# Kernel optimization log

Measured on AMD Instinct MI355X. Metric: run time of the kernel, lower is better.

Reference implementation:

```python
import jax, jax.numpy as jnp
import numpy as np

N_NODES = 100000


def gcn_conv(x, src, dst, W, b, n):
    # PyG GCNConv: add self-loops, symmetric deg^-1/2 normalization,
    # linear transform, gather->scatter-add aggregation, + bias.
    loop = jnp.arange(n, dtype=src.dtype)
    s = jnp.concatenate([src, loop])
    d = jnp.concatenate([dst, loop])
    deg = jax.ops.segment_sum(jnp.ones_like(d, dtype=x.dtype), d, num_segments=n)
    dinv = jnp.where(deg > 0, jax.lax.rsqrt(deg), jnp.zeros_like(deg))
    norm = dinv[s] * dinv[d]            # [E+N]
    h = x @ W                            # [N, out] (transform before propagate)
    msg = h[s] * norm[:, None]           # gather + scale
    out = jax.ops.segment_sum(msg, d, num_segments=n)  # scatter-add to dst
    return out + b


def setup_inputs() -> dict:
    key = jax.random.key(0)
    k = jax.random.split(key, 6)
    n, e, c_in, hid, c_out = N_NODES, 2500000, 5, 32, 1
    x = jax.random.normal(k[0], (n, c_in), dtype=jnp.float32)
    edge_index = jax.random.randint(k[1], (2, e), 0, n, dtype=jnp.int64)
    # Glorot-style init for GCN weights, zero bias (PyG default)
    W1 = jax.random.normal(k[2], (c_in, hid), dtype=jnp.float32) * (1.0 / np.sqrt(c_in))
    b1 = jnp.zeros((hid,), dtype=jnp.float32)
    W2 = jax.random.normal(k[3], (hid, c_out), dtype=jnp.float32) * (1.0 / np.sqrt(hid))
    b2 = jnp.zeros((c_out,), dtype=jnp.float32)
    return {"x": x, "edge_index": edge_index, "W1": W1, "b1": b1, "W2": W2, "b2": b2}


def reference(x, edge_index, W1, b1, W2, b2):
    n = x.shape[0]
    src, dst = edge_index[0], edge_index[1]
    h = jax.nn.relu(gcn_conv(x, src, dst, W1, b1, n))
    # dropout p=0.3 is identity at inference (training=False)
    return jax.nn.sigmoid(gcn_conv(h, src, dst, W2, b2, n))
```

## Files before the change

### kernel.cpp

```cpp
#include <hip/hip_runtime.h>
#include <math.h>


#define NB_SHIFT  8
#define BNODES    256
#define NBK       512
#define CAP       8192
#define CAP_SHIFT 13
#define CHUNK     4888
#define PBLK      512
#define RPT       16

struct SMemP0 {
    int sp[CHUNK];
    unsigned short sb[CHUNK];
    int cnt[NBK], ofs[NBK], cur[NBK], gbase[NBK];
    int wtmp[8];
};
struct SMemP1 {
    int stage2[CAP];
    int ofs[BNODES], cnt[BNODES], cur[BNODES];
    float w1[160], bb1[32], w2[32];
    int wtmp[8];
};
union SMem { SMemP0 p0; SMemP1 p1; };

__device__ __forceinline__ void gbar_arrive(int* bar, int tid) {
    __syncthreads();
    if (tid == 0) {
        __threadfence();
        __hip_atomic_fetch_add(bar, 1, __ATOMIC_RELAXED,
                               __HIP_MEMORY_SCOPE_AGENT);
    }
}
__device__ __forceinline__ void gbar_wait(int* bar, int tgt, int tid) {
    if (tid == 0) {
        while (__hip_atomic_load(bar, __ATOMIC_RELAXED,
                                 __HIP_MEMORY_SCOPE_AGENT) < tgt)
            __builtin_amdgcn_s_sleep(1);
        __threadfence();
    }
    __syncthreads();
}

__global__ __launch_bounds__(PBLK, 4) void k_fused(
        const int* __restrict__ src, const int* __restrict__ dst, int E,
        const float* __restrict__ x,
        const float* __restrict__ W1, const float* __restrict__ b1,
        const float* __restrict__ W2, const float* __restrict__ b2,
        float* __restrict__ out,
        int* __restrict__ pairs, int* __restrict__ bcur, int* __restrict__ gbar,
        float* __restrict__ h2s, float* __restrict__ xs, int n, int nb) {
    __shared__ SMem sm;
    const int tid  = threadIdx.x;
    const int blk  = blockIdx.x;
    const int G    = gridDim.x;
    const int lane = tid & 63, wv = tid >> 6;
    const int nbase = blk << NB_SHIFT;

    {
        int base = blk * CHUNK;
        if (base < E) {
            int m = min(CHUNK, E - base);
            sm.p0.cnt[tid] = 0;
            __syncthreads();
            for (int i = tid; i < m; i += 2 * PBLK) {
                int i1 = i + PBLK;
                int k0 = dst[base + i] >> NB_SHIFT;
                int k1 = (i1 < m) ? (dst[base + i1] >> NB_SHIFT) : -1;
                atomicAdd(&sm.p0.cnt[k0], 1);
                if (k1 >= 0) atomicAdd(&sm.p0.cnt[k1], 1);
            }
            __syncthreads();
            int v = sm.p0.cnt[tid];
            int s = v;
#pragma unroll
            for (int d = 1; d < 64; d <<= 1) {
                int t = __shfl_up(s, d);
                if (lane >= d) s += t;
            }
            if (lane == 63) sm.p0.wtmp[wv] = s;
            __syncthreads();
            if (wv == 0) {
                int t = (lane < 8) ? sm.p0.wtmp[lane] : 0;
#pragma unroll
                for (int d = 1; d < 8; d <<= 1) {
                    int u = __shfl_up(t, d);
                    if (lane >= d) t += u;
                }
                if (lane < 8) sm.p0.wtmp[lane] = t;
            }
            __syncthreads();
            int pre = s + (wv ? sm.p0.wtmp[wv - 1] : 0) - v;
            sm.p0.ofs[tid] = pre;
            sm.p0.cur[tid] = pre;
            sm.p0.gbase[tid] = (tid << CAP_SHIFT)
                             + (v ? atomicAdd(&bcur[tid], v) : 0);
            __syncthreads();
            for (int i = tid; i < m; i += 4 * PBLK) {
                int ia = i + PBLK, ib = i + 2 * PBLK, ic = i + 3 * PBLK;
                int s0 = src[base + i], d0 = dst[base + i];
                int s1 = 0, d1 = 0, s2 = 0, d2 = 0, s3 = 0, d3 = 0;
                if (ia < m) { s1 = src[base + ia]; d1 = dst[base + ia]; }
                if (ib < m) { s2 = src[base + ib]; d2 = dst[base + ib]; }
                if (ic < m) { s3 = src[base + ic]; d3 = dst[base + ic]; }
                int b0 = d0 >> NB_SHIFT;
                int p0 = atomicAdd(&sm.p0.cur[b0], 1);
                sm.p0.sp[p0] = ((d0 & (BNODES - 1)) << 24) | s0;
                sm.p0.sb[p0] = (unsigned short)b0;
                if (ia < m) {
                    int b1k = d1 >> NB_SHIFT;
                    int p1 = atomicAdd(&sm.p0.cur[b1k], 1);
                    sm.p0.sp[p1] = ((d1 & (BNODES - 1)) << 24) | s1;
                    sm.p0.sb[p1] = (unsigned short)b1k;
                }
                if (ib < m) {
                    int b2k = d2 >> NB_SHIFT;
                    int p2 = atomicAdd(&sm.p0.cur[b2k], 1);
                    sm.p0.sp[p2] = ((d2 & (BNODES - 1)) << 24) | s2;
                    sm.p0.sb[p2] = (unsigned short)b2k;
                }
                if (ic < m) {
                    int b3k = d3 >> NB_SHIFT;
                    int p3 = atomicAdd(&sm.p0.cur[b3k], 1);
                    sm.p0.sp[p3] = ((d3 & (BNODES - 1)) << 24) | s3;
                    sm.p0.sb[p3] = (unsigned short)b3k;
                }
            }
            __syncthreads();
            for (int i = tid; i < m; i += PBLK) {
                int b = sm.p0.sb[i];
                pairs[sm.p0.gbase[b] + (i - sm.p0.ofs[b])] = sm.p0.sp[i];
            }
        }
    }
    gbar_arrive(gbar, tid);
    float xr0 = 0.f, xr1 = 0.f, xr2 = 0.f, xr3 = 0.f, xr4 = 0.f;
    if (blk < nb) {
        if (tid < 160) sm.p1.w1[tid] = W1[tid];
        else if (tid < 192) sm.p1.bb1[tid - 160] = b1[tid - 160];
        else if (tid < 224) sm.p1.w2[tid - 192] = W2[tid - 192];
        if (tid < BNODES) {
            sm.p1.cnt[tid] = 0;
            int node = nbase + tid;
            if (node < n) {
                const float* xp = x + (size_t)node * 5;
                xr0 = xp[0]; xr1 = xp[1]; xr2 = xp[2]; xr3 = xp[3]; xr4 = xp[4];
            }
        }
    }
    gbar_wait(gbar, G, tid);

    int nrec = 0;
    int rec[RPT];
    if (blk < nb) {
        int base = blk << CAP_SHIFT;
        int len = min(((volatile int*)bcur)[blk], CAP);
#pragma unroll
        for (int j = 0; j < RPT; ++j) {
            int i = tid + j * PBLK;
            if (i < len) { rec[j] = pairs[base + i]; nrec = j + 1; }
        }
#pragma unroll
        for (int j = 0; j < RPT; ++j)
            if (j < nrec) atomicAdd(&sm.p1.cnt[((unsigned)rec[j]) >> 24], 1);
        __syncthreads();
        int v = (tid < BNODES) ? sm.p1.cnt[tid] : 0;
        int s = v;
#pragma unroll
        for (int d = 1; d < 64; d <<= 1) {
            int t = __shfl_up(s, d);
            if (lane >= d) s += t;
        }
        if (lane == 63 && wv < 4) sm.p1.wtmp[wv] = s;
        __syncthreads();
        if (wv == 0) {
            int t = (lane < 4) ? sm.p1.wtmp[lane] : 0;
#pragma unroll
            for (int d = 1; d < 4; d <<= 1) {
                int u = __shfl_up(t, d);
                if (lane >= d) t += u;
            }
            if (lane < 4) sm.p1.wtmp[lane] = t;
        }
        __syncthreads();
        if (tid < BNODES) {
            int pre = s + (wv ? sm.p1.wtmp[wv - 1] : 0) - v;
            sm.p1.ofs[tid] = pre;
            sm.p1.cur[tid] = pre;
            int node = nbase + tid;
            if (node < n) {
                float di = rsqrtf((float)v + 1.0f);
                float* xo = xs + ((size_t)node << 3);
                xo[0] = xr0 * di; xo[1] = xr1 * di; xo[2] = xr2 * di;
                xo[3] = xr3 * di; xo[4] = xr4 * di;
            }
        }
    }
    gbar_arrive(gbar, tid);
    if (blk < nb) {
#pragma unroll
        for (int j = 0; j < RPT; ++j)
            if (j < nrec) {
                int p = atomicAdd(&sm.p1.cur[((unsigned)rec[j]) >> 24], 1);
                sm.p1.stage2[p] = rec[j] & 0x00FFFFFF;
            }
    }
    gbar_wait(gbar, 2 * G, tid);

    if (blk < nb) {
        int t2 = tid >> 1, half = tid & 1;
        int node = nbase + t2;
        if (node < n) {
            int beg = sm.p1.ofs[t2], dg = sm.p1.cnt[t2];
            float a0 = 0.f, a1 = 0.f, a2 = 0.f, a3 = 0.f, a4 = 0.f;
            if (!half) {
                const float* xo = xs + ((size_t)node << 3);
                a0 = xo[0]; a1 = xo[1]; a2 = xo[2]; a3 = xo[3]; a4 = xo[4];
            }
            for (int e = beg + half; e < beg + dg; e += 2) {
                int sidx = sm.p1.stage2[e];
                const float* xr = xs + ((size_t)sidx << 3);
                float4 q = *(const float4*)xr;
                float q4 = xr[4];
                a0 += q.x; a1 += q.y; a2 += q.z; a3 += q.w; a4 += q4;
            }
            a0 += __shfl_xor(a0, 1); a1 += __shfl_xor(a1, 1);
            a2 += __shfl_xor(a2, 1); a3 += __shfl_xor(a3, 1);
            a4 += __shfl_xor(a4, 1);
            if (!half) {
                float di = rsqrtf((float)dg + 1.0f);
                a0 *= di; a1 *= di; a2 *= di; a3 *= di; a4 *= di;
                float sum = 0.f;
#pragma unroll
                for (int c = 0; c < 32; ++c) {
                    float z = sm.p1.bb1[c] + a0 * sm.p1.w1[c]
                            + a1 * sm.p1.w1[32 + c] + a2 * sm.p1.w1[64 + c]
                            + a3 * sm.p1.w1[96 + c] + a4 * sm.p1.w1[128 + c];
                    sum += fmaxf(z, 0.f) * sm.p1.w2[c];
                }
                h2s[node] = sum * di;
            }
        }
    }
    gbar_arrive(gbar, tid);
    gbar_wait(gbar, 3 * G, tid);

    if (blk < nb) {
        int t2 = tid >> 1, half = tid & 1;
        int node = nbase + t2;
        if (node >= n) return;
        int beg = sm.p1.ofs[t2], dg = sm.p1.cnt[t2];
        float a = 0.f;
        for (int e = beg + half; e < beg + dg; e += 2)
            a += h2s[sm.p1.stage2[e]];
        a += __shfl_xor(a, 1);
        if (!half) {
            float di = rsqrtf((float)dg + 1.0f);
            float vv = di * (a + h2s[node]) + b2[0];
            out[node] = 1.0f / (1.0f + __expf(-vv));
        }
    }
}


__global__ __launch_bounds__(512) void k_part(const int* __restrict__ src,
                                              const int* __restrict__ dst, int E,
                                              int* __restrict__ bcur,
                                              int* __restrict__ pairs) {
    __shared__ int sp[CHUNK];
    __shared__ unsigned short sb[CHUNK];
    __shared__ int cnt[NBK], ofs[NBK], cur[NBK], gbase[NBK];
    int tid = threadIdx.x;
    int base = blockIdx.x * CHUNK;
    int m = min(CHUNK, E - base);

    if (tid < NBK) cnt[tid] = 0;
    __syncthreads();
    for (int i = tid; i < m; i += 2 * 512) {
        int i1 = i + 512;
        int k0 = dst[base + i] >> NB_SHIFT;
        int k1 = (i1 < m) ? (dst[base + i1] >> NB_SHIFT) : -1;
        atomicAdd(&cnt[k0], 1);
        if (k1 >= 0) atomicAdd(&cnt[k1], 1);
    }
    __syncthreads();
    int v = cnt[tid];
    ofs[tid] = v;
    __syncthreads();
    for (int off = 1; off < NBK; off <<= 1) {
        int u = (tid >= off) ? ofs[tid - off] : 0;
        __syncthreads();
        ofs[tid] += u;
        __syncthreads();
    }
    int pre = ofs[tid] - v;
    ofs[tid] = pre;
    cur[tid] = pre;
    gbase[tid] = (tid << CAP_SHIFT) + (v ? atomicAdd(&bcur[tid], v) : 0);
    __syncthreads();
    for (int i = tid; i < m; i += 4 * 512) {
        int ia = i + 512, ib = i + 1024, ic = i + 1536;
        int s0 = src[base + i], d0 = dst[base + i];
        int s1 = 0, d1 = 0, s2 = 0, d2 = 0, s3 = 0, d3 = 0;
        if (ia < m) { s1 = src[base + ia]; d1 = dst[base + ia]; }
        if (ib < m) { s2 = src[base + ib]; d2 = dst[base + ib]; }
        if (ic < m) { s3 = src[base + ic]; d3 = dst[base + ic]; }
        int b0 = d0 >> NB_SHIFT;
        int p0 = atomicAdd(&cur[b0], 1);
        sp[p0] = ((d0 & (BNODES - 1)) << 24) | s0;
        sb[p0] = (unsigned short)b0;
        if (ia < m) {
            int b1 = d1 >> NB_SHIFT;
            int p1 = atomicAdd(&cur[b1], 1);
            sp[p1] = ((d1 & (BNODES - 1)) << 24) | s1;
            sb[p1] = (unsigned short)b1;
        }
        if (ib < m) {
            int b2 = d2 >> NB_SHIFT;
            int p2 = atomicAdd(&cur[b2], 1);
            sp[p2] = ((d2 & (BNODES - 1)) << 24) | s2;
            sb[p2] = (unsigned short)b2;
        }
        if (ic < m) {
            int b3 = d3 >> NB_SHIFT;
            int p3 = atomicAdd(&cur[b3], 1);
            sp[p3] = ((d3 & (BNODES - 1)) << 24) | s3;
            sb[p3] = (unsigned short)b3;
        }
    }
    __syncthreads();
    for (int i = tid; i < m; i += 512) {
        int b = sb[i];
        pairs[gbase[b] + (i - ofs[b])] = sp[i];
    }
}

__global__ __launch_bounds__(512) void k_sorta(const int* __restrict__ pairs,
                                               const int* __restrict__ bcur,
                                               const float* __restrict__ x,
                                               float* __restrict__ dinv,
                                               float* __restrict__ xs,
                                               int* __restrict__ nofs,
                                               int* __restrict__ deg, int n) {
    __shared__ int cnt[BNODES], scn[BNODES];
    int tid = threadIdx.x;
    int b = blockIdx.x;
    int base = b << CAP_SHIFT;
    int len = min(bcur[b], CAP);

    if (tid < BNODES) cnt[tid] = 0;
    __syncthreads();
    for (int i = tid; i < len; i += 512)
        atomicAdd(&cnt[((unsigned)pairs[base + i]) >> 24], 1);
    __syncthreads();
    int v = (tid < BNODES) ? cnt[tid] : 0;
    if (tid < BNODES) scn[tid] = v;
    __syncthreads();
    for (int off = 1; off < BNODES; off <<= 1) {
        int u = (tid < BNODES && tid >= off) ? scn[tid - off] : 0;
        __syncthreads();
        if (tid < BNODES) scn[tid] += u;
        __syncthreads();
    }
    if (tid < BNODES) {
        int node = (b << NB_SHIFT) + tid;
        if (node < n) {
            nofs[node] = base + scn[tid] - v;
            deg[node] = v;
            float di = rsqrtf((float)v + 1.0f);
            dinv[node] = di;
            const float* xr = x + (size_t)node * 5;
            float* xo = xs + ((size_t)node << 3);
#pragma unroll
            for (int k = 0; k < 5; ++k) xo[k] = xr[k] * di;
        }
    }
}

__global__ __launch_bounds__(512) void k_sortagg1(int* __restrict__ pairs,
                                                  const int* __restrict__ bcur,
                                                  const int* __restrict__ nofs,
                                                  const int* __restrict__ deg,
                                                  const float* __restrict__ xs,
                                                  const float* __restrict__ dinv,
                                                  const float* __restrict__ W1,
                                                  const float* __restrict__ b1,
                                                  const float* __restrict__ W2,
                                                  float* __restrict__ h2s, int n) {
    __shared__ int stage2[CAP];
    __shared__ int ofs[BNODES], cnt[BNODES], cur[BNODES];
    __shared__ float w1[160], bb1[32], w2[32];
    int tid = threadIdx.x;
    int b = blockIdx.x;
    int nbase = b << NB_SHIFT;
    int base = b << CAP_SHIFT;
    int len = min(bcur[b], CAP);

    if (tid < 160) w1[tid] = W1[tid];
    else if (tid < 192) bb1[tid - 160] = b1[tid - 160];
    else if (tid < 224) w2[tid - 192] = W2[tid - 192];
    if (tid < BNODES) {
        int node = nbase + tid;
        int o = 0, c = 0;
        if (node < n) { o = nofs[node] - base; c = deg[node]; }
        ofs[tid] = o; cnt[tid] = c; cur[tid] = o;
    }
    __syncthreads();
    for (int i = tid; i < len; i += 2048) {
        int ia = i + 512, ib = i + 1024, ic = i + 1536;
        int v0 = pairs[base + i];
        int v1 = (ia < len) ? pairs[base + ia] : -1;
        int v2 = (ib < len) ? pairs[base + ib] : -1;
        int v3 = (ic < len) ? pairs[base + ic] : -1;
        int p0 = atomicAdd(&cur[((unsigned)v0) >> 24], 1);
        stage2[p0] = v0 & 0x00FFFFFF;
        if (v1 != -1) {
            int p1 = atomicAdd(&cur[((unsigned)v1) >> 24], 1);
            stage2[p1] = v1 & 0x00FFFFFF;
        }
        if (v2 != -1) {
            int p2 = atomicAdd(&cur[((unsigned)v2) >> 24], 1);
            stage2[p2] = v2 & 0x00FFFFFF;
        }
        if (v3 != -1) {
            int p3 = atomicAdd(&cur[((unsigned)v3) >> 24], 1);
            stage2[p3] = v3 & 0x00FFFFFF;
        }
    }
    __syncthreads();
    {
        int len4 = len >> 2;
        const int4* s4 = (const int4*)stage2;
        int4* p4 = (int4*)(pairs + base);
        for (int i = tid; i < len4; i += 512) p4[i] = s4[i];
        for (int i = (len4 << 2) + tid; i < len; i += 512)
            pairs[base + i] = stage2[i];
    }
    int t2 = tid >> 1, half = tid & 1;
    int node = nbase + t2;
    if (node >= n) return;
    int beg = ofs[t2], dg = cnt[t2];
    float a0 = 0.f, a1 = 0.f, a2 = 0.f, a3 = 0.f, a4 = 0.f;
    if (!half) {
        const float* xo = xs + ((size_t)node << 3);
        a0 = xo[0]; a1 = xo[1]; a2 = xo[2]; a3 = xo[3]; a4 = xo[4];
    }
    for (int e = beg + half; e < beg + dg; e += 2) {
        int s = stage2[e];
        const float* xr = xs + ((size_t)s << 3);
        float4 q = *(const float4*)xr;
        float q4 = xr[4];
        a0 += q.x; a1 += q.y; a2 += q.z; a3 += q.w; a4 += q4;
    }
    a0 += __shfl_xor(a0, 1); a1 += __shfl_xor(a1, 1); a2 += __shfl_xor(a2, 1);
    a3 += __shfl_xor(a3, 1); a4 += __shfl_xor(a4, 1);
    if (half) return;
    float di = dinv[node];
    a0 *= di; a1 *= di; a2 *= di; a3 *= di; a4 *= di;
    float sum = 0.f;
#pragma unroll
    for (int c = 0; c < 32; ++c) {
        float z = bb1[c] + a0 * w1[c] + a1 * w1[32 + c] + a2 * w1[64 + c]
                         + a3 * w1[96 + c] + a4 * w1[128 + c];
        sum += fmaxf(z, 0.f) * w2[c];
    }
    h2s[node] = sum * di;
}

__global__ __launch_bounds__(256) void k_agg2(const int* __restrict__ pairs,
                                              const int* __restrict__ nofs,
                                              const int* __restrict__ deg,
                                              const float* __restrict__ h2s,
                                              const float* __restrict__ dinv,
                                              const float* __restrict__ b2,
                                              float* __restrict__ out, int n) {
    int tid = threadIdx.x;
    int node = blockIdx.x * 64 + (tid >> 2);
    int q = tid & 3;
    if (node >= n) return;
    int beg = nofs[node], dg = deg[node];
    float a = 0.f;
    for (int e = beg + q; e < beg + dg; e += 4) a += h2s[pairs[e]];
    a += __shfl_xor(a, 1);
    a += __shfl_xor(a, 2);
    if (q) return;
    float v = dinv[node] * (a + h2s[node]) + b2[0];
    out[node] = 1.0f / (1.0f + __expf(-v));
}

extern "C" void kernel_launch(void* const* d_in, const int* in_sizes, int n_in,
                              void* d_out, int out_size, void* d_ws, size_t ws_size,
                              hipStream_t stream) {
    const float* x  = (const float*)d_in[0];
    const int*   ei = (const int*)d_in[1];
    const float* W1 = (const float*)d_in[2];
    const float* b1 = (const float*)d_in[3];
    const float* W2 = (const float*)d_in[4];
    const float* b2 = (const float*)d_in[5];
    float* out = (float*)d_out;

    const int n = in_sizes[0] / 5;
    const int E = in_sizes[1] / 2;
    const int* src = ei;
    const int* dst = ei + E;
    const int nb = (n + BNODES - 1) >> NB_SHIFT;

    int* wsi = (int*)d_ws;
    int*   pairs = wsi;
    int*   bcur  = wsi + ((size_t)(nb + 1) << CAP_SHIFT);
    int*   gbar  = bcur + NBK;
    int*   deg   = gbar + 16;
    int*   nofs  = deg + n;
    float* dinv  = (float*)(nofs + n);
    float* h2s   = dinv + n;
    float* xs    = h2s + n;

    const int nchunk = (E + CHUNK - 1) / CHUNK;
    const int g = nchunk > nb ? nchunk : nb;

    static int use_coop = -1;
    if (use_coop < 0) {
        int dev = 0, ncu = 0, maxb = 0;
        hipGetDevice(&dev);
        hipDeviceGetAttribute(&ncu, hipDeviceAttributeMultiprocessorCount, dev);
        hipError_t e = hipOccupancyMaxActiveBlocksPerMultiprocessor(
                &maxb, k_fused, PBLK, 0);
        int coop = 0;
        hipDeviceGetAttribute(&coop, hipDeviceAttributeCooperativeLaunch, dev);
        use_coop = (e == hipSuccess && coop && (long)maxb * ncu >= g) ? 1 : 0;
    }

    hipMemsetAsync(bcur, 0, (NBK + 16) * sizeof(int), stream);

    if (use_coop) {
        void* args[] = {(void*)&src, (void*)&dst, (void*)&E, (void*)&x,
                        (void*)&W1, (void*)&b1, (void*)&W2, (void*)&b2,
                        (void*)&out, (void*)&pairs, (void*)&bcur, (void*)&gbar,
                        (void*)&h2s, (void*)&xs, (void*)&n, (void*)&nb};
        hipError_t e = hipLaunchCooperativeKernel((const void*)k_fused,
                                                  dim3(g), dim3(PBLK),
                                                  args, 0, stream);
        if (e == hipSuccess) return;
        use_coop = 0;
    }

    const int nagg = (n + 63) / 64;
    k_part<<<nchunk, 512, 0, stream>>>(src, dst, E, bcur, pairs);
    k_sorta<<<nb, 512, 0, stream>>>(pairs, bcur, x, dinv, xs, nofs, deg, n);
    k_sortagg1<<<nb, 512, 0, stream>>>(pairs, bcur, nofs, deg, xs, dinv,
                                       W1, b1, W2, h2s, n);
    k_agg2<<<nagg, 256, 0, stream>>>(pairs, nofs, deg, h2s, dinv, b2, out, n);
}
```

Measured before the change: 143.7 us.

## Vectorize edge and pair loads with int4 and shard grid barrier counter

Edge src/dst chunks and per-bucket pair records are now loaded as int4 vectors into registers up front instead of scalar strided loads, cutting the number of global load instructions in the partition and sort phases. The single global barrier counter is split into 8 padded counters so arriving blocks contend on separate cache lines, while waiters sum all 8. The int4 loads need 16-byte alignment of the chunk bases; CHUNK=4888 and CAP are multiples of 4, so this holds if the inputs are aligned. Polling now reads eight locations per spin iteration.

```diff
diff --git a/kernel.cpp b/kernel.cpp
--- a/kernel.cpp
+++ b/kernel.cpp
@@ -9,7 +9,9 @@
 #define CAP_SHIFT 13
 #define CHUNK     4888
 #define PBLK      512
-#define RPT       16
+#define RPT0      3
+#define RPT4      4
+#define GBS       16
 
 struct SMemP0 {
     int sp[CHUNK];
@@ -25,19 +27,25 @@
 };
 union SMem { SMemP0 p0; SMemP1 p1; };
 
-__device__ __forceinline__ void gbar_arrive(int* bar, int tid) {
+__device__ __forceinline__ void gbar_arrive(int* bar, int blk, int tid) {
     __syncthreads();
     if (tid == 0) {
         __threadfence();
-        __hip_atomic_fetch_add(bar, 1, __ATOMIC_RELAXED,
+        __hip_atomic_fetch_add(&bar[(blk & 7) * GBS], 1, __ATOMIC_RELAXED,
                                __HIP_MEMORY_SCOPE_AGENT);
     }
 }
 __device__ __forceinline__ void gbar_wait(int* bar, int tgt, int tid) {
     if (tid == 0) {
-        while (__hip_atomic_load(bar, __ATOMIC_RELAXED,
-                                 __HIP_MEMORY_SCOPE_AGENT) < tgt)
+        for (;;) {
+            int s = 0;
+#pragma unroll
+            for (int k = 0; k < 8; ++k)
+                s += __hip_atomic_load(&bar[k * GBS], __ATOMIC_RELAXED,
+                                       __HIP_MEMORY_SCOPE_AGENT);
+            if (s >= tgt) break;
             __builtin_amdgcn_s_sleep(1);
+        }
         __threadfence();
     }
     __syncthreads();
@@ -62,15 +70,29 @@
         int base = blk * CHUNK;
         if (base < E) {
             int m = min(CHUNK, E - base);
+            int m4 = m >> 2;
+            int4 dv[RPT0], sv[RPT0];
+            int nv = 0;
+            const int4* d4 = (const int4*)(dst + base);
+            const int4* s4g = (const int4*)(src + base);
+#pragma unroll
+            for (int j = 0; j < RPT0; ++j) {
+                int idx = tid + j * PBLK;
+                if (idx < m4) { dv[j] = d4[idx]; sv[j] = s4g[idx]; nv = j + 1; }
+            }
+            int tb = (m4 << 2) + tid;
+            int td = 0, ts = 0, tvalid = 0;
+            if (tb < m) { td = dst[base + tb]; ts = src[base + tb]; tvalid = 1; }
             sm.p0.cnt[tid] = 0;
             __syncthreads();
-            for (int i = tid; i < m; i += 2 * PBLK) {
-                int i1 = i + PBLK;
-                int k0 = dst[base + i] >> NB_SHIFT;
-                int k1 = (i1 < m) ? (dst[base + i1] >> NB_SHIFT) : -1;
-                atomicAdd(&sm.p0.cnt[k0], 1);
-                if (k1 >= 0) atomicAdd(&sm.p0.cnt[k1], 1);
-            }
+#pragma unroll
+            for (int j = 0; j < RPT0; ++j) if (j < nv) {
+                atomicAdd(&sm.p0.cnt[dv[j].x >> NB_SHIFT], 1);
+                atomicAdd(&sm.p0.cnt[dv[j].y >> NB_SHIFT], 1);
+                atomicAdd(&sm.p0.cnt[dv[j].z >> NB_SHIFT], 1);
+                atomicAdd(&sm.p0.cnt[dv[j].w >> NB_SHIFT], 1);
+            }
+            if (tvalid) atomicAdd(&sm.p0.cnt[td >> NB_SHIFT], 1);
             __syncthreads();
             int v = sm.p0.cnt[tid];
             int s = v;
@@ -97,35 +119,27 @@
             sm.p0.gbase[tid] = (tid << CAP_SHIFT)
                              + (v ? atomicAdd(&bcur[tid], v) : 0);
             __syncthreads();
-            for (int i = tid; i < m; i += 4 * PBLK) {
-                int ia = i + PBLK, ib = i + 2 * PBLK, ic = i + 3 * PBLK;
-                int s0 = src[base + i], d0 = dst[base + i];
-                int s1 = 0, d1 = 0, s2 = 0, d2 = 0, s3 = 0, d3 = 0;
-                if (ia < m) { s1 = src[base + ia]; d1 = dst[base + ia]; }
-                if (ib < m) { s2 = src[base + ib]; d2 = dst[base + ib]; }
-                if (ic < m) { s3 = src[base + ic]; d3 = dst[base + ic]; }
-                int b0 = d0 >> NB_SHIFT;
-                int p0 = atomicAdd(&sm.p0.cur[b0], 1);
-                sm.p0.sp[p0] = ((d0 & (BNODES - 1)) << 24) | s0;
-                sm.p0.sb[p0] = (unsigned short)b0;
-                if (ia < m) {
-                    int b1k = d1 >> NB_SHIFT;
-                    int p1 = atomicAdd(&sm.p0.cur[b1k], 1);
-                    sm.p0.sp[p1] = ((d1 & (BNODES - 1)) << 24) | s1;
-                    sm.p0.sb[p1] = (unsigned short)b1k;
-                }
-                if (ib < m) {
-                    int b2k = d2 >> NB_SHIFT;
-                    int p2 = atomicAdd(&sm.p0.cur[b2k], 1);
-                    sm.p0.sp[p2] = ((d2 & (BNODES - 1)) << 24) | s2;
-                    sm.p0.sb[p2] = (unsigned short)b2k;
-                }
-                if (ic < m) {
-                    int b3k = d3 >> NB_SHIFT;
-                    int p3 = atomicAdd(&sm.p0.cur[b3k], 1);
-                    sm.p0.sp[p3] = ((d3 & (BNODES - 1)) << 24) | s3;
-                    sm.p0.sb[p3] = (unsigned short)b3k;
-                }
+#pragma unroll
+            for (int j = 0; j < RPT0; ++j) if (j < nv) {
+                int b, p;
+                b = dv[j].x >> NB_SHIFT; p = atomicAdd(&sm.p0.cur[b], 1);
+                sm.p0.sp[p] = ((dv[j].x & (BNODES - 1)) << 24) | sv[j].x;
+                sm.p0.sb[p] = (unsigned short)b;
+                b = dv[j].y >> NB_SHIFT; p = atomicAdd(&sm.p0.cur[b], 1);
+                sm.p0.sp[p] = ((dv[j].y & (BNODES - 1)) << 24) | sv[j].y;
+                sm.p0.sb[p] = (unsigned short)b;
+                b = dv[j].z >> NB_SHIFT; p = atomicAdd(&sm.p0.cur[b], 1);
+                sm.p0.sp[p] = ((dv[j].z & (BNODES - 1)) << 24) | sv[j].z;
+                sm.p0.sb[p] = (unsigned short)b;
+                b = dv[j].w >> NB_SHIFT; p = atomicAdd(&sm.p0.cur[b], 1);
+                sm.p0.sp[p] = ((dv[j].w & (BNODES - 1)) << 24) | sv[j].w;
+                sm.p0.sb[p] = (unsigned short)b;
+            }
+            if (tvalid) {
+                int b = td >> NB_SHIFT;
+                int p = atomicAdd(&sm.p0.cur[b], 1);
+                sm.p0.sp[p] = ((td & (BNODES - 1)) << 24) | ts;
+                sm.p0.sb[p] = (unsigned short)b;
             }
             __syncthreads();
             for (int i = tid; i < m; i += PBLK) {
@@ -134,7 +148,7 @@
             }
         }
     }
-    gbar_arrive(gbar, tid);
+    gbar_arrive(gbar, blk, tid);
     float xr0 = 0.f, xr1 = 0.f, xr2 = 0.f, xr3 = 0.f, xr4 = 0.f;
     if (blk < nb) {
         if (tid < 160) sm.p1.w1[tid] = W1[tid];
@@ -151,19 +165,28 @@
     }
     gbar_wait(gbar, G, tid);
 
-    int nrec = 0;
-    int rec[RPT];
+    int4 rc[RPT4];
+    int nv4 = 0, rt = 0, rtv = 0;
     if (blk < nb) {
         int base = blk << CAP_SHIFT;
         int len = min(((volatile int*)bcur)[blk], CAP);
-#pragma unroll
-        for (int j = 0; j < RPT; ++j) {
-            int i = tid + j * PBLK;
-            if (i < len) { rec[j] = pairs[base + i]; nrec = j + 1; }
-        }
-#pragma unroll
-        for (int j = 0; j < RPT; ++j)
-            if (j < nrec) atomicAdd(&sm.p1.cnt[((unsigned)rec[j]) >> 24], 1);
+        int len4 = len >> 2;
+        const int4* p4 = (const int4*)(pairs + base);
+#pragma unroll
+        for (int j = 0; j < RPT4; ++j) {
+            int idx = tid + j * PBLK;
+            if (idx < len4) { rc[j] = p4[idx]; nv4 = j + 1; }
+        }
+        int i = (len4 << 2) + tid;
+        if (i < len) { rt = pairs[base + i]; rtv = 1; }
+#pragma unroll
+        for (int j = 0; j < RPT4; ++j) if (j < nv4) {
+            atomicAdd(&sm.p1.cnt[((unsigned)rc[j].x) >> 24], 1);
+            atomicAdd(&sm.p1.cnt[((unsigned)rc[j].y) >> 24], 1);
+            atomicAdd(&sm.p1.cnt[((unsigned)rc[j].z) >> 24], 1);
+            atomicAdd(&sm.p1.cnt[((unsigned)rc[j].w) >> 24], 1);
+        }
+        if (rtv) atomicAdd(&sm.p1.cnt[((unsigned)rt) >> 24], 1);
         __syncthreads();
         int v = (tid < BNODES) ? sm.p1.cnt[tid] : 0;
         int s = v;
@@ -197,14 +220,24 @@
             }
         }
     }
-    gbar_arrive(gbar, tid);
+    gbar_arrive(gbar, blk, tid);
     if (blk < nb) {
 #pragma unroll
-        for (int j = 0; j < RPT; ++j)
-            if (j < nrec) {
-                int p = atomicAdd(&sm.p1.cur[((unsigned)rec[j]) >> 24], 1);
-                sm.p1.stage2[p] = rec[j] & 0x00FFFFFF;
-            }
+        for (int j = 0; j < RPT4; ++j) if (j < nv4) {
+            int p;
+            p = atomicAdd(&sm.p1.cur[((unsigned)rc[j].x) >> 24], 1);
+            sm.p1.stage2[p] = rc[j].x & 0x00FFFFFF;
+            p = atomicAdd(&sm.p1.cur[((unsigned)rc[j].y) >> 24], 1);
+            sm.p1.stage2[p] = rc[j].y & 0x00FFFFFF;
+            p = atomicAdd(&sm.p1.cur[((unsigned)rc[j].z) >> 24], 1);
+            sm.p1.stage2[p] = rc[j].z & 0x00FFFFFF;
+            p = atomicAdd(&sm.p1.cur[((unsigned)rc[j].w) >> 24], 1);
+            sm.p1.stage2[p] = rc[j].w & 0x00FFFFFF;
+        }
+        if (rtv) {
+            int p = atomicAdd(&sm.p1.cur[((unsigned)rt) >> 24], 1);
+            sm.p1.stage2[p] = rt & 0x00FFFFFF;
+        }
     }
     gbar_wait(gbar, 2 * G, tid);
 
@@ -243,7 +276,7 @@
             }
         }
     }
-    gbar_arrive(gbar, tid);
+    gbar_arrive(gbar, blk, tid);
     gbar_wait(gbar, 3 * G, tid);
 
     if (blk < nb) {
@@ -510,7 +543,7 @@
     int*   pairs = wsi;
     int*   bcur  = wsi + ((size_t)(nb + 1) << CAP_SHIFT);
     int*   gbar  = bcur + NBK;
-    int*   deg   = gbar + 16;
+    int*   deg   = gbar + 8 * GBS;
     int*   nofs  = deg + n;
     float* dinv  = (float*)(nofs + n);
     float* h2s   = dinv + n;
@@ -531,7 +564,7 @@
         use_coop = (e == hipSuccess && coop && (long)maxb * ncu >= g) ? 1 : 0;
     }
 
-    hipMemsetAsync(bcur, 0, (NBK + 16) * sizeof(int), stream);
+    hipMemsetAsync(bcur, 0, (NBK + 8 * GBS) * sizeof(int), stream);
 
     if (use_coop) {
         void* args[] = {(void*)&src, (void*)&dst, (void*)&E, (void*)&x,
```

New measurement: 141.6 us. About the same (-1.4%).
